# Performance work log

Hardware: AMD Instinct MI355X
Metric: run time of the kernel (lower is better)

Reference implementation:

```python
import jax, jax.numpy as jnp
import numpy as np

B, N, E, C, ND, MID, OUT = 4, 16384, 131072, 128, 3, 128, 128


def setup_inputs() -> dict:
    key = jax.random.key(0)
    ks = jax.random.split(key, 11)
    f = jax.random.normal(ks[0], (B, C, N), dtype=jnp.float32)
    nodes = jax.random.normal(ks[1], (B, N, ND), dtype=jnp.float32)
    node_weights = jax.random.uniform(ks[2], (B, N, 1), dtype=jnp.float32)  # positive quadrature weights
    edges_index = jax.random.randint(ks[3], (B, E, 2), 0, N)
    edge_gradient_weights = jax.random.normal(ks[4], (B, E, ND), dtype=jnp.float32) * 0.1
    mlp_w1 = jax.random.normal(ks[5], (MID, ND * C), dtype=jnp.float32) * 0.02
    mlp_b1 = jnp.zeros((MID,), dtype=jnp.float32)
    mlp_w2 = jax.random.normal(ks[6], (OUT, MID), dtype=jnp.float32) * 0.02
    mlp_b2 = jnp.zeros((OUT,), dtype=jnp.float32)
    L = jax.random.normal(ks[7], (ND, ND), dtype=jnp.float32) * 0.1  # Cholesky factor (scaled for non-degenerate exp)
    chol_bias = jnp.zeros((ND,), dtype=jnp.float32)
    return dict(f=f, nodes=nodes, node_weights=node_weights, edges_index=edges_index,
                edge_gradient_weights=edge_gradient_weights, mlp_w1=mlp_w1, mlp_b1=mlp_b1,
                mlp_w2=mlp_w2, mlp_b2=mlp_b2, L=L, chol_bias=chol_bias)


def reference(f, nodes, node_weights, edges_index, edge_gradient_weights,
              mlp_w1, mlp_b1, mlp_w2, mlp_b2, L, chol_bias):
    b, c, n = f.shape
    nd = edge_gradient_weights.shape[-1]
    bidx = jnp.arange(b)[:, None]
    src_g = edges_index[..., 0]
    tgt_g = edges_index[..., 1]

    # ---- compute_gradient: gather f[src]-f[tgt], weight by edge_gradient_weights, scatter-add to target ----
    fT = f.transpose(0, 2, 1)  # (B,N,C)
    df = jnp.take_along_axis(fT, src_g[..., None], axis=1) - jnp.take_along_axis(fT, tgt_g[..., None], axis=1)  # (B,E,C)
    msg = (df[:, :, :, None] * edge_gradient_weights[:, :, None, :]).reshape(b, df.shape[1], c * nd)  # 'bed,bec->becd'
    grad = jnp.zeros((b, n, c * nd), f.dtype).at[bidx, tgt_g].add(msg)
    g = grad.transpose(0, 2, 1)  # (B, C*nd, N)

    # ---- pointwise MLP over channel dim (Conv1d k=1 -> GELU -> Conv1d k=1) ----
    h = jnp.einsum('mk,bkn->bmn', mlp_w1, g) + mlp_b1[None, :, None]
    h = jax.nn.gelu(h, approximate=False)
    h = jnp.einsum('om,bmn->bon', mlp_w2, h) + mlp_b2[None, :, None]
    fo = h.transpose(0, 2, 1)  # (B,N,OUT)
    o = fo.shape[-1]

    # ---- Gaussian edge kernel via Cholesky PSD form, with self-edges appended ----
    self_e = jnp.broadcast_to(jnp.arange(n)[None, :], (b, n))
    src = jnp.concatenate([src_g, self_e], axis=-1)
    tgt = jnp.concatenate([tgt_g, self_e], axis=-1)
    f_src = jnp.take_along_axis(fo, src[..., None], axis=1)  # (B,E+N,OUT)
    d = jnp.take_along_axis(nodes, src[..., None], axis=1) - jnp.take_along_axis(nodes, tgt[..., None], axis=1)  # (B,E+N,nd)
    Sigma = L @ L.T  # positive semi-definite inverse covariance
    dS = d @ Sigma.T + chol_bias  # F.linear
    w_src = jnp.take_along_axis(node_weights, src[..., None], axis=1)[..., 0]  # (B,E+N)
    kernel = w_src * jnp.exp(-jnp.einsum('bed,bed->be', d, dS))

    # ---- scatter-add normalization and aggregation ----
    inv = 1.0 / jnp.zeros((b, n), f.dtype).at[bidx, tgt].add(kernel)
    out = jnp.zeros((b, n, o), f.dtype).at[bidx, tgt].add(f_src * kernel[..., None]) * inv[..., None]
    return out.transpose(0, 2, 1)  # (B,OUT,N)
```

## Files before the change

### kernel.cpp

```cpp
#include <hip/hip_runtime.h>
#include <hip/hip_bf16.h>

static constexpr int B   = 4;
static constexpr int N   = 16384;
static constexpr int E   = 131072;
static constexpr int C   = 128;
static constexpr int ND  = 3;
static constexpr int MID = 128;
static constexpr int OUT = 128;
static constexpr int K1  = C * ND;
static constexpr int NT  = 32;
static constexpr int K1P = 392;

typedef __attribute__((ext_vector_type(8))) short bf16x8;
typedef __attribute__((ext_vector_type(4))) float f32x4;

__device__ __forceinline__ ushort f2bf(float x) {
    union { float f; unsigned u; } v; v.f = x;
    return (ushort)((v.u + 0x7fffu + ((v.u >> 16) & 1u)) >> 16);
}
__device__ __forceinline__ float bf2f(ushort u) {
    union { unsigned u; float f; } v; v.u = (unsigned)u << 16;
    return v.f;
}

__global__ void k_prep(const float* __restrict__ W1, const float* __restrict__ W2,
                       const float* __restrict__ L, ushort* __restrict__ W1p,
                       ushort* __restrict__ W2p, float* __restrict__ Sig) {
    int gid = blockIdx.x * 256 + threadIdx.x;
    for (int i = gid; i < 8 * 12 * 64 * 8; i += 64 * 256) {
        int j = i & 7, l = (i >> 3) & 63, t = (i >> 9) % 12, nt = (i >> 9) / 12;
        int n = nt * 16 + (l & 15);
        int k = t * 32 + ((l >> 4) & 3) * 8 + j;
        W1p[i] = f2bf(W1[n * K1 + k]);
    }
    for (int i = gid; i < 8 * 4 * 64 * 8; i += 64 * 256) {
        int j = i & 7, l = (i >> 3) & 63, t = (i >> 9) % 4, nt = (i >> 9) / 4;
        int n = nt * 16 + (l & 15);
        int k = t * 32 + ((l >> 4) & 3) * 8 + j;
        W2p[i] = f2bf(W2[n * MID + k]);
    }
    if (gid < 9) {
        int i = gid / 3, j = gid % 3;
        Sig[gid] = L[i * 3 + 0] * L[j * 3 + 0] + L[i * 3 + 1] * L[j * 3 + 1] +
                   L[i * 3 + 2] * L[j * 3 + 2];
    }
}

__global__ void k_transpose(const float* __restrict__ f, ushort* __restrict__ fT) {
    __shared__ float tile[32][33];
    int b = blockIdx.z;
    int n0 = blockIdx.x * 32, c0 = blockIdx.y * 32;
    const float* fb = f + (size_t)b * C * N;
    ushort* fTb = fT + (size_t)b * N * C;
    int tx = threadIdx.x, ty = threadIdx.y;
    #pragma unroll
    for (int i = 0; i < 32; i += 8)
        tile[ty + i][tx] = fb[(size_t)(c0 + ty + i) * N + n0 + tx];
    __syncthreads();
    #pragma unroll
    for (int i = 0; i < 32; i += 8)
        fTb[(size_t)(n0 + ty + i) * C + c0 + tx] = f2bf(tile[tx][ty + i]);
}

__global__ void k_count(const int2* __restrict__ ei2, int* __restrict__ deg) {
    int idx = blockIdx.x * 256 + threadIdx.x;
    int b = idx >> 17;
    int tgt = ei2[idx].y;
    atomicAdd(&deg[b * N + tgt], 1);
}

__global__ void k_scan1(const int4* __restrict__ degv, int* __restrict__ rowptr,
                        int* __restrict__ bsum) {
    __shared__ int s[256];
    int blk = blockIdx.x, t = threadIdx.x;
    int4 d = degv[blk * 256 + t];
    s[t] = d.x + d.y + d.z + d.w;
    __syncthreads();
    for (int off = 1; off < 256; off <<= 1) {
        int v = s[t];
        int u = (t >= off) ? s[t - off] : 0;
        __syncthreads();
        s[t] = v + u;
        __syncthreads();
    }
    int excl = (t == 0) ? 0 : s[t - 1];
    if (t == 255) bsum[blk] = s[255];
    int4 w;
    w.x = excl;
    w.y = excl + d.x;
    w.z = w.y + d.y;
    w.w = w.z + d.z;
    ((int4*)rowptr)[blk * 256 + t] = w;
}

__global__ void k_scan2(int* __restrict__ bsum, int* __restrict__ rowptr) {
    __shared__ int s[64];
    int t = threadIdx.x;
    s[t] = bsum[t];
    __syncthreads();
    for (int off = 1; off < 64; off <<= 1) {
        int v = s[t];
        int u = (t >= off) ? s[t - off] : 0;
        __syncthreads();
        s[t] = v + u;
        __syncthreads();
    }
    bsum[t] = (t == 0) ? 0 : s[t - 1];
    if (t == 63) rowptr[B * N] = s[63];
}

__global__ void k_scan3(int4* __restrict__ rowv, const int* __restrict__ bsum) {
    int i = blockIdx.x * 256 + threadIdx.x;
    int add = bsum[i >> 8];
    int4 v = rowv[i];
    v.x += add; v.y += add; v.z += add; v.w += add;
    rowv[i] = v;
}

__global__ void k_fill_perm(const int2* __restrict__ ei2,
                            const int* __restrict__ rowptr,
                            int* __restrict__ cursor, int* __restrict__ perm) {
    int idx = blockIdx.x * 256 + threadIdx.x;
    int b = idx >> 17;
    int tgt = ei2[idx].y;
    int bn = b * N + tgt;
    int pos = atomicAdd(&cursor[bn], 1);
    perm[rowptr[bn] + pos] = idx;
}

__global__ void k_fill_expand(const int* __restrict__ perm,
                              const int2* __restrict__ ei2,
                              const float* __restrict__ egw,
                              const float* __restrict__ nodes,
                              const float* __restrict__ nw,
                              const float* __restrict__ Sig,
                              const float* __restrict__ cb,
                              float4* __restrict__ egwp, float2* __restrict__ ka2) {
    int o = blockIdx.x * 256 + threadIdx.x;
    int idx = perm[o];
    int b = idx >> 17;
    int2 e = ei2[idx];
    int src = e.x, tgt = e.y;
    const float* w = egw + (size_t)idx * ND;
    egwp[o] = make_float4(w[0], w[1], w[2], __int_as_float(src));
    const float* ns = nodes + ((size_t)b * N + src) * ND;
    const float* nt = nodes + ((size_t)b * N + tgt) * ND;
    float d0 = ns[0] - nt[0], d1 = ns[1] - nt[1], d2 = ns[2] - nt[2];
    float q = d0 * (Sig[0] * d0 + Sig[1] * d1 + Sig[2] * d2) +
              d1 * (Sig[3] * d0 + Sig[4] * d1 + Sig[5] * d2) +
              d2 * (Sig[6] * d0 + Sig[7] * d1 + Sig[8] * d2) +
              d0 * cb[0] + d1 * cb[1] + d2 * cb[2];
    ka2[o] = make_float2(nw[(size_t)b * N + src] * expf(-q), __int_as_float(src));
}

#define EDGE_FMA(W, U)                                                         \
    {                                                                          \
        float dx = bf2f(U.x) - ft.x, dy = bf2f(U.y) - ft.y,                    \
              dz = bf2f(U.z) - ft.z, dw = bf2f(U.w) - ft.w;                    \
        a0.x = fmaf(dx, W.x, a0.x); a0.y = fmaf(dy, W.x, a0.y);                \
        a0.z = fmaf(dz, W.x, a0.z); a0.w = fmaf(dw, W.x, a0.w);                \
        a1.x = fmaf(dx, W.y, a1.x); a1.y = fmaf(dy, W.y, a1.y);                \
        a1.z = fmaf(dz, W.y, a1.z); a1.w = fmaf(dw, W.y, a1.w);                \
        a2.x = fmaf(dx, W.z, a2.x); a2.y = fmaf(dy, W.z, a2.y);                \
        a2.z = fmaf(dz, W.z, a2.z); a2.w = fmaf(dw, W.z, a2.w);                \
    }

__global__ __launch_bounds__(512, 5) void k_grad_mlp(
    const ushort* __restrict__ fT, const int* __restrict__ rowptr,
    const float4* __restrict__ egwp, const ushort* __restrict__ W1p,
    const float* __restrict__ b1, const ushort* __restrict__ W2p,
    const float* __restrict__ b2, ushort* __restrict__ fo) {
    __shared__ ushort g_s[NT][K1P];
    int tid = threadIdx.x;
    int n0 = blockIdx.x * NT;

    {
        int cg = tid & 31, s = tid >> 5;
        int cg4 = cg * 4;
        for (int jj = 0; jj < NT; jj += 16) {
            int j = jj + s;
            int n = n0 + j;
            const ushort* fTb = fT + (size_t)(n >> 14) * N * C;
            float4 ft;
            {
                ushort4 u = *(const ushort4*)(fT + (size_t)n * C + cg4);
                ft = make_float4(bf2f(u.x), bf2f(u.y), bf2f(u.z), bf2f(u.w));
            }
            int base = rowptr[n], cnt = rowptr[n + 1] - base;
            float4 a0 = make_float4(0.f, 0.f, 0.f, 0.f), a1 = a0, a2 = a0;
            int i = 0;
            for (; i + 4 <= cnt; i += 4) {
                float4 w0 = egwp[base + i];
                float4 w1 = egwp[base + i + 1];
                float4 w2 = egwp[base + i + 2];
                float4 w3 = egwp[base + i + 3];
                ushort4 u0 = *(const ushort4*)(fTb + (size_t)__float_as_int(w0.w) * C + cg4);
                ushort4 u1 = *(const ushort4*)(fTb + (size_t)__float_as_int(w1.w) * C + cg4);
                ushort4 u2 = *(const ushort4*)(fTb + (size_t)__float_as_int(w2.w) * C + cg4);
                ushort4 u3 = *(const ushort4*)(fTb + (size_t)__float_as_int(w3.w) * C + cg4);
                EDGE_FMA(w0, u0);
                EDGE_FMA(w1, u1);
                EDGE_FMA(w2, u2);
                EDGE_FMA(w3, u3);
            }
            for (; i < cnt; ++i) {
                float4 w0 = egwp[base + i];
                ushort4 u0 = *(const ushort4*)(fTb + (size_t)__float_as_int(w0.w) * C + cg4);
                EDGE_FMA(w0, u0);
            }
            unsigned p0 = (unsigned)f2bf(a0.x) | ((unsigned)f2bf(a1.x) << 16);
            unsigned p1 = (unsigned)f2bf(a2.x) | ((unsigned)f2bf(a0.y) << 16);
            unsigned p2 = (unsigned)f2bf(a1.y) | ((unsigned)f2bf(a2.y) << 16);
            unsigned p3 = (unsigned)f2bf(a0.z) | ((unsigned)f2bf(a1.z) << 16);
            unsigned p4 = (unsigned)f2bf(a2.z) | ((unsigned)f2bf(a0.w) << 16);
            unsigned p5 = (unsigned)f2bf(a1.w) | ((unsigned)f2bf(a2.w) << 16);
            uint2* dst = (uint2*)&g_s[j][cg * 12];
            dst[0] = make_uint2(p0, p1);
            dst[1] = make_uint2(p2, p3);
            dst[2] = make_uint2(p4, p5);
        }
    }
    __syncthreads();

    int wv = tid >> 6, ln = tid & 63, lr = ln & 15, lh = ln >> 4;
    int mt = wv & 1, nh = wv >> 1;
    bf16x8 a[12];
    {
        const ushort* grow = &g_s[mt * 16 + lr][0];
        #pragma unroll
        for (int t = 0; t < 12; ++t)
            a[t] = *(const bf16x8*)(grow + t * 32 + lh * 8);
    }
    __syncthreads();

    ushort(*h_s)[136] = (ushort(*)[136]) & g_s[0][0];
    const bf16x8* W1f = (const bf16x8*)W1p;
    #pragma unroll
    for (int q = 0; q < 2; ++q) {
        int nt = nh * 2 + q;
        float bb = b1[nt * 16 + lr];
        f32x4 c = {bb, bb, bb, bb};
        #pragma unroll
        for (int t = 0; t < 12; ++t)
            c = __builtin_amdgcn_mfma_f32_16x16x32_bf16(
                a[t], W1f[(nt * 12 + t) * 64 + ln], c, 0, 0, 0);
        #pragma unroll
        for (int r = 0; r < 4; ++r) {
            float x = c[r];
            x = 0.5f * x * (1.0f + erff(x * 0.70710678118654752f));
            h_s[mt * 16 + lh * 4 + r][nt * 16 + lr] = f2bf(x);
        }
    }
    __syncthreads();

    bf16x8 a2[4];
    {
        const ushort* hrow = &h_s[mt * 16 + lr][0];
        #pragma unroll
        for (int t = 0; t < 4; ++t)
            a2[t] = *(const bf16x8*)(hrow + t * 32 + lh * 8);
    }
    const bf16x8* W2f = (const bf16x8*)W2p;
    #pragma unroll
    for (int q = 0; q < 2; ++q) {
        int nt = nh * 2 + q;
        float bb = b2[nt * 16 + lr];
        f32x4 c = {bb, bb, bb, bb};
        #pragma unroll
        for (int t = 0; t < 4; ++t)
            c = __builtin_amdgcn_mfma_f32_16x16x32_bf16(
                a2[t], W2f[(nt * 4 + t) * 64 + ln], c, 0, 0, 0);
        #pragma unroll
        for (int r = 0; r < 4; ++r)
            fo[(size_t)(n0 + mt * 16 + lh * 4 + r) * OUT + nt * 16 + lr] = f2bf(c[r]);
    }
}

#define AGG_FMA(K, U)                                                          \
    {                                                                          \
        o.x = fmaf(bf2f(U.x), K.x, o.x); o.y = fmaf(bf2f(U.y), K.x, o.y);      \
        o.z = fmaf(bf2f(U.z), K.x, o.z); o.w = fmaf(bf2f(U.w), K.x, o.w);      \
        den += K.x;                                                            \
    }

__global__ __launch_bounds__(512, 5) void k_agg_t(const ushort* __restrict__ fo,
                                                  const float* __restrict__ nw,
                                                  const int* __restrict__ rowptr,
                                                  const float2* __restrict__ ka2,
                                                  float* __restrict__ out) {
    __shared__ float t[OUT][65];
    int tid = threadIdx.x;
    int cg4 = (tid & 31) * 4;
    int s = tid >> 5;
    int n0 = blockIdx.x * 64;
    int b = n0 >> 14, ncol0 = n0 & (N - 1);
    const ushort* fob = fo + (size_t)b * N * OUT;
    for (int g = 0; g < 4; ++g) {
        int nl = g * 16 + s;
        int n = n0 + nl;
        int base = rowptr[n], cnt = rowptr[n + 1] - base;
        float4 o = make_float4(0.f, 0.f, 0.f, 0.f);
        float den = 0.f;
        int i = 0;
        for (; i + 4 <= cnt; i += 4) {
            float2 k0 = ka2[base + i];
            float2 k1 = ka2[base + i + 1];
            float2 k2 = ka2[base + i + 2];
            float2 k3 = ka2[base + i + 3];
            ushort4 u0 = *(const ushort4*)(fob + (size_t)__float_as_int(k0.y) * OUT + cg4);
            ushort4 u1 = *(const ushort4*)(fob + (size_t)__float_as_int(k1.y) * OUT + cg4);
            ushort4 u2 = *(const ushort4*)(fob + (size_t)__float_as_int(k2.y) * OUT + cg4);
            ushort4 u3 = *(const ushort4*)(fob + (size_t)__float_as_int(k3.y) * OUT + cg4);
            AGG_FMA(k0, u0);
            AGG_FMA(k1, u1);
            AGG_FMA(k2, u2);
            AGG_FMA(k3, u3);
        }
        for (; i < cnt; ++i) {
            float2 k0 = ka2[base + i];
            ushort4 u0 = *(const ushort4*)(fob + (size_t)__float_as_int(k0.y) * OUT + cg4);
            AGG_FMA(k0, u0);
        }
        float wn = nw[n];
        ushort4 uf = *(const ushort4*)(fo + (size_t)n * OUT + cg4);
        float inv = 1.f / (den + wn);
        t[cg4 + 0][nl] = (o.x + bf2f(uf.x) * wn) * inv;
        t[cg4 + 1][nl] = (o.y + bf2f(uf.y) * wn) * inv;
        t[cg4 + 2][nl] = (o.z + bf2f(uf.z) * wn) * inv;
        t[cg4 + 3][nl] = (o.w + bf2f(uf.w) * wn) * inv;
    }
    __syncthreads();
    #pragma unroll
    for (int i = 0; i < 16; ++i) {
        int idx = tid + i * 512;
        int o = idx >> 6, nl = idx & 63;
        out[((size_t)b * OUT + o) * N + ncol0 + nl] = t[o][nl];
    }
}

extern "C" void kernel_launch(void* const* d_in, const int* in_sizes, int n_in,
                              void* d_out, int out_size, void* d_ws, size_t ws_size,
                              hipStream_t stream) {
    const float* f     = (const float*)d_in[0];
    const float* nodes = (const float*)d_in[1];
    const float* nw    = (const float*)d_in[2];
    const int*   ei    = (const int*)d_in[3];
    const float* egw   = (const float*)d_in[4];
    const float* W1    = (const float*)d_in[5];
    const float* b1    = (const float*)d_in[6];
    const float* W2    = (const float*)d_in[7];
    const float* b2    = (const float*)d_in[8];
    const float* L     = (const float*)d_in[9];
    const float* cb    = (const float*)d_in[10];
    float* out = (float*)d_out;

    char* ws = (char*)d_ws;
    auto alloc = [&](size_t bytes) {
        void* p = ws;
        ws += (bytes + 255) & ~(size_t)255;
        return p;
    };
    ushort* fT     = (ushort*)alloc((size_t)B * N * C * 2);
    ushort* fo     = (ushort*)alloc((size_t)B * N * OUT * 2);
    ushort* W1p    = (ushort*)alloc((size_t)MID * K1 * 2);
    ushort* W2p    = (ushort*)alloc((size_t)OUT * MID * 2);
    float*  Sig    = (float*)alloc(16 * 4);
    int*    deg    = (int*)alloc((size_t)B * N * 4);
    int*    cursor = (int*)alloc((size_t)B * N * 4);
    int*    rowptr = (int*)alloc(((size_t)B * N + 4) * 4);
    int*    bsum   = (int*)alloc(64 * 4);
    int*    perm   = (int*)alloc((size_t)B * E * 4);
    float4* egwp   = (float4*)alloc((size_t)B * E * 16);
    float2* ka2    = (float2*)alloc((size_t)B * E * 8);

    hipMemsetAsync(deg, 0, (size_t)B * N * 4, stream);
    hipMemsetAsync(cursor, 0, (size_t)B * N * 4, stream);

    k_prep<<<64, 256, 0, stream>>>(W1, W2, L, W1p, W2p, Sig);
    k_transpose<<<dim3(N / 32, C / 32, B), dim3(32, 8), 0, stream>>>(f, fT);
    k_count<<<(B * E) / 256, 256, 0, stream>>>((const int2*)ei, deg);
    k_scan1<<<64, 256, 0, stream>>>((const int4*)deg, rowptr, bsum);
    k_scan2<<<1, 64, 0, stream>>>(bsum, rowptr);
    k_scan3<<<64, 256, 0, stream>>>((int4*)rowptr, bsum);
    k_fill_perm<<<(B * E) / 256, 256, 0, stream>>>((const int2*)ei, rowptr, cursor,
                                                   perm);
    k_fill_expand<<<(B * E) / 256, 256, 0, stream>>>(perm, (const int2*)ei, egw,
                                                     nodes, nw, Sig, cb, egwp, ka2);
    k_grad_mlp<<<(B * N) / NT, 512, 0, stream>>>(fT, rowptr, egwp, W1p, b1, W2p,
                                                 b2, fo);
    k_agg_t<<<(B * N) / 64, 512, 0, stream>>>(fo, nw, rowptr, ka2, out);
}
```

Baseline: 171.6 us.

## Merge front kernels, swizzle block order, store MLP output as fp32

Merges the prep, transpose and degree-count kernels into one launch that dispatches by block index, and replaces the two memsets with a single one over contiguous deg/cursor buffers. It also swizzles the block-to-node mapping in the grad-MLP and aggregation kernels, and keeps the MLP output fo in fp32 instead of bf16. The aim is to cut launch overhead and bf16 conversions and to improve locality, at the cost of doubling fo traffic in the gather-heavy aggregation. The single memset depends on cursor sitting directly after deg in the workspace.

New measurement: 168.8 us. No clear change (-1.6%).

```diff
diff --git a/kernel.cpp b/kernel.cpp
--- a/kernel.cpp
+++ b/kernel.cpp
@@ -24,50 +24,52 @@
     return v.f;
 }
 
-__global__ void k_prep(const float* __restrict__ W1, const float* __restrict__ W2,
-                       const float* __restrict__ L, ushort* __restrict__ W1p,
-                       ushort* __restrict__ W2p, float* __restrict__ Sig) {
-    int gid = blockIdx.x * 256 + threadIdx.x;
-    for (int i = gid; i < 8 * 12 * 64 * 8; i += 64 * 256) {
-        int j = i & 7, l = (i >> 3) & 63, t = (i >> 9) % 12, nt = (i >> 9) / 12;
-        int n = nt * 16 + (l & 15);
-        int k = t * 32 + ((l >> 4) & 3) * 8 + j;
-        W1p[i] = f2bf(W1[n * K1 + k]);
-    }
-    for (int i = gid; i < 8 * 4 * 64 * 8; i += 64 * 256) {
-        int j = i & 7, l = (i >> 3) & 63, t = (i >> 9) % 4, nt = (i >> 9) / 4;
-        int n = nt * 16 + (l & 15);
-        int k = t * 32 + ((l >> 4) & 3) * 8 + j;
-        W2p[i] = f2bf(W2[n * MID + k]);
-    }
-    if (gid < 9) {
-        int i = gid / 3, j = gid % 3;
-        Sig[gid] = L[i * 3 + 0] * L[j * 3 + 0] + L[i * 3 + 1] * L[j * 3 + 1] +
-                   L[i * 3 + 2] * L[j * 3 + 2];
-    }
-}
-
-__global__ void k_transpose(const float* __restrict__ f, ushort* __restrict__ fT) {
+__global__ void k_front(const float* __restrict__ f, ushort* __restrict__ fT,
+                        const int2* __restrict__ ei2, int* __restrict__ deg,
+                        const float* __restrict__ W1, const float* __restrict__ W2,
+                        const float* __restrict__ L, ushort* __restrict__ W1p,
+                        ushort* __restrict__ W2p, float* __restrict__ Sig) {
     __shared__ float tile[32][33];
-    int b = blockIdx.z;
-    int n0 = blockIdx.x * 32, c0 = blockIdx.y * 32;
-    const float* fb = f + (size_t)b * C * N;
-    ushort* fTb = fT + (size_t)b * N * C;
-    int tx = threadIdx.x, ty = threadIdx.y;
-    #pragma unroll
-    for (int i = 0; i < 32; i += 8)
-        tile[ty + i][tx] = fb[(size_t)(c0 + ty + i) * N + n0 + tx];
-    __syncthreads();
-    #pragma unroll
-    for (int i = 0; i < 32; i += 8)
-        fTb[(size_t)(n0 + ty + i) * C + c0 + tx] = f2bf(tile[tx][ty + i]);
-}
-
-__global__ void k_count(const int2* __restrict__ ei2, int* __restrict__ deg) {
-    int idx = blockIdx.x * 256 + threadIdx.x;
-    int b = idx >> 17;
-    int tgt = ei2[idx].y;
-    atomicAdd(&deg[b * N + tgt], 1);
+    int bid = blockIdx.x, tid = threadIdx.x;
+    if (bid < 8192) {
+        int bx = bid & 511, by = (bid >> 9) & 3, b = bid >> 11;
+        int n0 = bx * 32, c0 = by * 32;
+        const float* fb = f + (size_t)b * C * N;
+        ushort* fTb = fT + (size_t)b * N * C;
+        int tx = tid & 31, ty = tid >> 5;
+        #pragma unroll
+        for (int i = 0; i < 32; i += 8)
+            tile[ty + i][tx] = fb[(size_t)(c0 + ty + i) * N + n0 + tx];
+        __syncthreads();
+        #pragma unroll
+        for (int i = 0; i < 32; i += 8)
+            fTb[(size_t)(n0 + ty + i) * C + c0 + tx] = f2bf(tile[tx][ty + i]);
+    } else if (bid < 10240) {
+        int idx = (bid - 8192) * 256 + tid;
+        int b = idx >> 17;
+        int tgt = ei2[idx].y;
+        atomicAdd(&deg[b * N + tgt], 1);
+    } else {
+        int gid = (bid - 10240) * 256 + tid;
+        for (int i = gid; i < 8 * 12 * 64 * 8; i += 64 * 256) {
+            int j = i & 7, l = (i >> 3) & 63, t = (i >> 9) % 12, nt = (i >> 9) / 12;
+            int n = nt * 16 + (l & 15);
+            int k = t * 32 + ((l >> 4) & 3) * 8 + j;
+            W1p[i] = f2bf(W1[n * K1 + k]);
+        }
+        {
+            int i = gid;
+            int j = i & 7, l = (i >> 3) & 63, t = (i >> 9) % 4, nt = (i >> 9) / 4;
+            int n = nt * 16 + (l & 15);
+            int k = t * 32 + ((l >> 4) & 3) * 8 + j;
+            W2p[i] = f2bf(W2[n * MID + k]);
+        }
+        if (gid < 9) {
+            int i = gid / 3, j = gid % 3;
+            Sig[gid] = L[i * 3 + 0] * L[j * 3 + 0] + L[i * 3 + 1] * L[j * 3 + 1] +
+                       L[i * 3 + 2] * L[j * 3 + 2];
+        }
+    }
 }
 
 __global__ void k_scan1(const int4* __restrict__ degv, int* __restrict__ rowptr,
@@ -170,10 +172,12 @@
     const ushort* __restrict__ fT, const int* __restrict__ rowptr,
     const float4* __restrict__ egwp, const ushort* __restrict__ W1p,
     const float* __restrict__ b1, const ushort* __restrict__ W2p,
-    const float* __restrict__ b2, ushort* __restrict__ fo) {
+    const float* __restrict__ b2, float* __restrict__ fo) {
     __shared__ ushort g_s[NT][K1P];
     int tid = threadIdx.x;
-    int n0 = blockIdx.x * NT;
+    int bid = blockIdx.x;
+    int swz = (bid & 7) * ((B * N / NT) >> 3) + (bid >> 3);
+    int n0 = swz * NT;
 
     {
         int cg = tid & 31, s = tid >> 5;
@@ -273,18 +277,18 @@
                 a2[t], W2f[(nt * 4 + t) * 64 + ln], c, 0, 0, 0);
         #pragma unroll
         for (int r = 0; r < 4; ++r)
-            fo[(size_t)(n0 + mt * 16 + lh * 4 + r) * OUT + nt * 16 + lr] = f2bf(c[r]);
-    }
-}
-
-#define AGG_FMA(K, U)                                                          \
+            fo[(size_t)(n0 + mt * 16 + lh * 4 + r) * OUT + nt * 16 + lr] = c[r];
+    }
+}
+
+#define AGG_FMA(K, F)                                                          \
     {                                                                          \
-        o.x = fmaf(bf2f(U.x), K.x, o.x); o.y = fmaf(bf2f(U.y), K.x, o.y);      \
-        o.z = fmaf(bf2f(U.z), K.x, o.z); o.w = fmaf(bf2f(U.w), K.x, o.w);      \
+        o.x = fmaf(F.x, K.x, o.x); o.y = fmaf(F.y, K.x, o.y);                  \
+        o.z = fmaf(F.z, K.x, o.z); o.w = fmaf(F.w, K.x, o.w);                  \
         den += K.x;                                                            \
     }
 
-__global__ __launch_bounds__(512, 5) void k_agg_t(const ushort* __restrict__ fo,
+__global__ __launch_bounds__(512, 5) void k_agg_t(const float* __restrict__ fo,
                                                   const float* __restrict__ nw,
                                                   const int* __restrict__ rowptr,
                                                   const float2* __restrict__ ka2,
@@ -293,9 +297,12 @@
     int tid = threadIdx.x;
     int cg4 = (tid & 31) * 4;
     int s = tid >> 5;
-    int n0 = blockIdx.x * 64;
+    int bid = blockIdx.x;
+    int swz = (bid & 7) * ((B * N / 64) >> 3) + (bid >> 3);
+    int n0 = swz * 64;
     int b = n0 >> 14, ncol0 = n0 & (N - 1);
-    const ushort* fob = fo + (size_t)b * N * OUT;
+    const float* fob = fo + (size_t)b * N * OUT;
+    #pragma unroll
     for (int g = 0; g < 4; ++g) {
         int nl = g * 16 + s;
         int n = n0 + nl;
@@ -308,27 +315,27 @@
             float2 k1 = ka2[base + i + 1];
             float2 k2 = ka2[base + i + 2];
             float2 k3 = ka2[base + i + 3];
-            ushort4 u0 = *(const ushort4*)(fob + (size_t)__float_as_int(k0.y) * OUT + cg4);
-            ushort4 u1 = *(const ushort4*)(fob + (size_t)__float_as_int(k1.y) * OUT + cg4);
-            ushort4 u2 = *(const ushort4*)(fob + (size_t)__float_as_int(k2.y) * OUT + cg4);
-            ushort4 u3 = *(const ushort4*)(fob + (size_t)__float_as_int(k3.y) * OUT + cg4);
-            AGG_FMA(k0, u0);
-            AGG_FMA(k1, u1);
-            AGG_FMA(k2, u2);
-            AGG_FMA(k3, u3);
+            float4 f0 = *(const float4*)(fob + (size_t)__float_as_int(k0.y) * OUT + cg4);
+            float4 f1 = *(const float4*)(fob + (size_t)__float_as_int(k1.y) * OUT + cg4);
+            float4 f2 = *(const float4*)(fob + (size_t)__float_as_int(k2.y) * OUT + cg4);
+            float4 f3 = *(const float4*)(fob + (size_t)__float_as_int(k3.y) * OUT + cg4);
+            AGG_FMA(k0, f0);
+            AGG_FMA(k1, f1);
+            AGG_FMA(k2, f2);
+            AGG_FMA(k3, f3);
         }
         for (; i < cnt; ++i) {
             float2 k0 = ka2[base + i];
-            ushort4 u0 = *(const ushort4*)(fob + (size_t)__float_as_int(k0.y) * OUT + cg4);
-            AGG_FMA(k0, u0);
+            float4 f0 = *(const float4*)(fob + (size_t)__float_as_int(k0.y) * OUT + cg4);
+            AGG_FMA(k0, f0);
         }
         float wn = nw[n];
-        ushort4 uf = *(const ushort4*)(fo + (size_t)n * OUT + cg4);
+        float4 uf = *(const float4*)(fo + (size_t)n * OUT + cg4);
         float inv = 1.f / (den + wn);
-        t[cg4 + 0][nl] = (o.x + bf2f(uf.x) * wn) * inv;
-        t[cg4 + 1][nl] = (o.y + bf2f(uf.y) * wn) * inv;
-        t[cg4 + 2][nl] = (o.z + bf2f(uf.z) * wn) * inv;
-        t[cg4 + 3][nl] = (o.w + bf2f(uf.w) * wn) * inv;
+        t[cg4 + 0][nl] = (o.x + uf.x * wn) * inv;
+        t[cg4 + 1][nl] = (o.y + uf.y * wn) * inv;
+        t[cg4 + 2][nl] = (o.z + uf.z * wn) * inv;
+        t[cg4 + 3][nl] = (o.w + uf.w * wn) * inv;
     }
     __syncthreads();
     #pragma unroll
@@ -362,7 +369,7 @@
         return p;
     };
     ushort* fT     = (ushort*)alloc((size_t)B * N * C * 2);
-    ushort* fo     = (ushort*)alloc((size_t)B * N * OUT * 2);
+    float*  fo     = (float*)alloc((size_t)B * N * OUT * 4);
     ushort* W1p    = (ushort*)alloc((size_t)MID * K1 * 2);
     ushort* W2p    = (ushort*)alloc((size_t)OUT * MID * 2);
     float*  Sig    = (float*)alloc(16 * 4);
@@ -374,12 +381,10 @@
     float4* egwp   = (float4*)alloc((size_t)B * E * 16);
     float2* ka2    = (float2*)alloc((size_t)B * E * 8);
 
-    hipMemsetAsync(deg, 0, (size_t)B * N * 4, stream);
-    hipMemsetAsync(cursor, 0, (size_t)B * N * 4, stream);
-
-    k_prep<<<64, 256, 0, stream>>>(W1, W2, L, W1p, W2p, Sig);
-    k_transpose<<<dim3(N / 32, C / 32, B), dim3(32, 8), 0, stream>>>(f, fT);
-    k_count<<<(B * E) / 256, 256, 0, stream>>>((const int2*)ei, deg);
+    hipMemsetAsync(deg, 0, (size_t)B * N * 4 * 2, stream);
+
+    k_front<<<10304, 256, 0, stream>>>(f, fT, (const int2*)ei, deg, W1, W2, L,
+                                       W1p, W2p, Sig);
     k_scan1<<<64, 256, 0, stream>>>((const int4*)deg, rowptr, bsum);
     k_scan2<<<1, 64, 0, stream>>>(bsum, rowptr);
     k_scan3<<<64, 256, 0, stream>>>((int4*)rowptr, bsum);
```
